# Performance work log

Hardware: AMD Instinct MI355X
Metric: run time of the kernel (lower is better)

Reference implementation:

```python
import jax, jax.numpy as jnp
import numpy as np

BS, N, DX, DE, DY, NH = 4, 256, 256, 64, 128, 8
DF = DX // NH
ORDER = 3


def layer_norm(x, g, b, eps=1e-6):
    m = jnp.mean(x, -1, keepdims=True)
    v = jnp.mean((x - m) ** 2, -1, keepdims=True)
    return (x - m) / jnp.sqrt(v + eps) * g + b


def setup_inputs() -> dict:
    key = jax.random.key(0)
    ks = jax.random.split(key, 32)
    s = 0.02
    p = {}
    p['X'] = jax.random.normal(ks[0], (BS, N, DX), jnp.float32)
    p['E'] = jax.random.normal(ks[1], (BS, N, N, DE), jnp.float32)
    p['y'] = jax.random.normal(ks[2], (BS, DY), jnp.float32)
    lens = jax.random.randint(ks[3], (BS,), N // 2, N + 1)
    p['node_mask'] = (jnp.arange(N)[None, :] < lens[:, None]).astype(jnp.int32)
    p['W_emax'] = s * jax.random.normal(ks[4], (DE, DX))
    p['W_x1'] = s * jax.random.normal(ks[5], (DX, DX))
    p['Wq'] = s * jax.random.normal(ks[6], (DX, DX))
    p['Wk'] = s * jax.random.normal(ks[7], (DX, DX))
    p['Wv'] = s * jax.random.normal(ks[8], (DX, DX))
    p['Wo'] = s * jax.random.normal(ks[9], (DX, DX))
    p['W_y2'] = s * jax.random.normal(ks[10], (DY, DX))
    p['W_x2'] = s * jax.random.normal(ks[11], (DX, DX))
    p['Wc'] = s * jax.random.normal(ks[12], (DY, ORDER))
    p['bc'] = jnp.zeros((ORDER,), jnp.float32)
    p['sim_alpha'] = 0.1 * jax.random.normal(ks[13], (1,))
    p['W_Eout'] = s * jax.random.normal(ks[14], (DE, DE))
    p['G_kernel'] = 0.01 * jax.random.normal(ks[15], (DE, 128))
    p['X_kernel'] = 0.01 * jax.random.normal(ks[16], (DX, 64))
    p['W_Gtrans'] = s * jax.random.normal(ks[17], (128 * DE, DY))
    p['W_Xtrans'] = s * jax.random.normal(ks[18], (64 * DX, DY))
    p['W_yout'] = s * jax.random.normal(ks[19], (DY, DY))
    p['gx'] = jnp.ones((DX,), jnp.float32); p['bx'] = jnp.zeros((DX,), jnp.float32)
    p['ge'] = jnp.ones((DE,), jnp.float32); p['be'] = jnp.zeros((DE,), jnp.float32)
    p['gy'] = jnp.ones((DY,), jnp.float32); p['by'] = jnp.zeros((DY,), jnp.float32)
    return p


def reference(X, E, y, node_mask, W_emax, W_x1, Wq, Wk, Wv, Wo, W_y2, W_x2, Wc, bc,
              sim_alpha, W_Eout, G_kernel, X_kernel, W_Gtrans, W_Xtrans, W_yout,
              gx, bx, ge, be, gy, by):
    bs, n, dx = X.shape
    de = E.shape[-1]
    nm = node_mask.astype(X.dtype)              # bs, n
    x_mask = nm[:, :, None]                     # bs, n, 1
    emask = x_mask[:, :, None, :] * x_mask[:, None, :, :]  # bs, n, n, 1

    # --- edge -> node encoding (masked mean over dim 2; torch mean divides by n) ---
    e_enc = jax.nn.relu(jnp.mean(jnp.einsum('bijd,df->bijf', E, W_emax) * emask, axis=2))
    xplus = (X + jax.nn.relu(e_enc @ W_x1)) * x_mask

    # --- masked multi-head self attention (dropout = identity in eval) ---
    q = (xplus @ Wq).reshape(bs, n, NH, DF)
    k = (xplus @ Wk).reshape(bs, n, NH, DF)
    v = (xplus @ Wv).reshape(bs, n, NH, DF)
    scores = jnp.einsum('bqhd,bkhd->bhqk', q, k) / (DF ** 0.5)
    scores = jnp.where(nm[:, None, None, :] > 0, scores, -1e9)
    attn_out = jnp.einsum('bhqk,bkhd->bqhd', jax.nn.softmax(scores, -1), v).reshape(bs, n, dx) @ Wo
    new_X = layer_norm(attn_out * x_mask + X, gx, bx)

    # --- similarity-augmented edge matrix + order-3 polynomial recurrence ---
    xplusy = jax.nn.relu((X + jax.nn.relu(y @ W_y2)[:, None, :]) @ W_x2)
    sim = jnp.einsum('bnd,bmd->bnm', xplusy, xplusy) / (dx ** 0.5)
    G = (sim_alpha * sim[..., None] + E) * emask          # bs, n, n, de
    Gr = G.reshape(bs, de, n, n)                          # raw reshape, exactly as torch
    coeff = y @ Wc + bc                                    # bs, 3
    newE = coeff[:, 0][:, None, None, None] * Gr
    for kk in range(1, ORDER):
        newE = jnp.matmul(Gr, newE) + coeff[:, kk][:, None, None, None] * Gr
    new_E = layer_norm(jax.nn.relu(newE.reshape(bs, n, n, de) @ W_Eout) * emask + E, ge, be)

    # --- masked softmax pooling over edges ---
    Em = E * emask
    lg = jnp.where(emask > 0, (Em @ G_kernel) / (de ** 0.5), -1e9)   # bs,n,n,128
    aG = jax.nn.softmax(lg.reshape(bs, n * n, -1), axis=1)            # bs,n^2,128
    G_enc = jnp.einsum('bpk,bpd->bkd', aG, Em.reshape(bs, n * n, de)).reshape(bs, -1)
    G_enc = jax.nn.relu(G_enc @ W_Gtrans)

    # --- masked softmax pooling over nodes ---
    Xm = x_mask * X
    lx = jnp.where(x_mask > 0, (Xm @ X_kernel) / (dx ** 0.5), -1e9)   # bs,n,64
    aX = jax.nn.softmax(lx, axis=1)
    X_enc = jnp.einsum('bnk,bnd->bkd', aX, Xm).reshape(bs, -1)
    X_enc = jax.nn.relu(X_enc @ W_Xtrans)

    new_y = layer_norm(jax.nn.relu((G_enc + X_enc) @ W_yout) + y, gy, by)
    return new_X, new_E, new_y
```

## Files before the change

kernel.cpp:

```cpp
#include <hip/hip_runtime.h>
#include <hip/hip_bf16.h>

typedef __hip_bfloat16 bf16;
__device__ __forceinline__ bf16 tobf(float v){ return __float2bfloat16(v); }
__device__ __forceinline__ float frombf(bf16 v){ return __bfloat162float(v); }
__device__ __forceinline__ short f2bs(float x){ bf16 h=tobf(x); return *reinterpret_cast<short*>(&h); }
__device__ __forceinline__ float bs2f(short s){ unsigned int v=((unsigned int)(unsigned short)s)<<16; return __int_as_float((int)v); }

typedef __attribute__((ext_vector_type(8))) short bf16x8;
typedef __attribute__((ext_vector_type(4))) short short4v;
typedef __attribute__((ext_vector_type(4))) float f32x4;
typedef __attribute__((ext_vector_type(4))) int int4v;

static constexpr int cB=4, cN=256, cDX=256, cDE=64, cDY=128, cNH=8, cDF=32;

static constexpr size_t F_SIM  = 0;
static constexpr size_t F_P    = 262144;
static constexpr size_t F_NP   = 2359296;
static constexpr size_t F_GP   = F_NP + 1048576;
static constexpr size_t F_XP   = F_NP + 1048576 + 32768;
static constexpr size_t F_S    = 6619136;
static constexpr size_t F_EENC = 6684672;
static constexpr size_t F_XPL  = 6946816;
static constexpr size_t F_QB   = 7208960;
static constexpr size_t F_KB   = 7471104;
static constexpr size_t F_VB   = 7733248;
static constexpr size_t F_YW   = 7995392;
static constexpr size_t F_XPY  = 7996416;
static constexpr size_t F_COEF = 8258560;
static constexpr size_t F_GENC = 8258576;
static constexpr size_t F_XENC = 8291344;

__global__ void k_coeff_yw(const float* y, const float* Wc, const float* bc,
                           const float* W_y2, float* coeff, float* yw){
  int b = blockIdx.x; int f = threadIdx.x;
  float acc = 0.f;
  for(int r=0;r<cDY;++r) acc += y[b*cDY+r]*W_y2[r*cDX+f];
  yw[b*cDX+f] = fmaxf(acc,0.f);
  if (f < 3){
    float c = bc[f];
    for(int r=0;r<cDY;++r) c += y[b*cDY+r]*Wc[r*3+f];
    coeff[b*3+f] = c;
  }
}

__global__ void k_reduceE(const float* E, const int* nm, float* S){
  int bi = blockIdx.x; int b = bi / cN;
  int d = threadIdx.x;
  int jy = threadIdx.y;
  const float* Eb = E + (size_t)bi*cN*cDE;
  float acc = 0.f;
  for(int j=jy;j<cN;j+=4){
    acc += Eb[j*cDE+d] * (float)nm[b*cN+j];
  }
  __shared__ float red[4][64];
  red[jy][d]=acc; __syncthreads();
  if (jy==0) S[(size_t)bi*cDE+d] = red[0][d]+red[1][d]+red[2][d]+red[3][d];
}

__global__ void k_eenc(const float* S, const float* W_emax, const int* nm, float* eenc){
  int bi = blockIdx.x; int b = bi/cN; int i = bi%cN;
  int f = threadIdx.x;
  __shared__ float s[cDE];
  if (f<cDE) s[f]=S[(size_t)bi*cDE+f];
  __syncthreads();
  float acc=0.f;
  for(int d=0;d<cDE;++d) acc += s[d]*W_emax[d*cDX+f];
  float mi=(float)nm[b*cN+i];
  eenc[(size_t)bi*cDX+f] = fmaxf(acc*mi*(1.f/cN), 0.f);
}

__global__ void k_xplus(const float* X, const float* eenc, const float* W_x1,
                        const int* nm, float* xplus){
  int bi=blockIdx.x; int b=bi/cN; int i=bi%cN;
  int f=threadIdx.x;
  __shared__ float row[cDX];
  row[f]=eenc[(size_t)bi*cDX+f];
  __syncthreads();
  float acc=0.f;
  for(int c=0;c<cDX;++c) acc += row[c]*W_x1[c*cDX+f];
  float mi=(float)nm[b*cN+i];
  xplus[(size_t)bi*cDX+f] = (X[(size_t)bi*cDX+f] + fmaxf(acc,0.f))*mi;
}

__global__ void k_qkv(const float* xplus, const float* Wq, const float* Wk, const float* Wv,
                      float* qb, float* kb, float* vb){
  int bi=blockIdx.x; int f=threadIdx.x;
  __shared__ float row[cDX];
  row[f]=xplus[(size_t)bi*cDX+f];
  __syncthreads();
  float aq=0,ak=0,av=0;
  for(int c=0;c<cDX;++c){ float r=row[c]; aq+=r*Wq[c*cDX+f]; ak+=r*Wk[c*cDX+f]; av+=r*Wv[c*cDX+f]; }
  qb[(size_t)bi*cDX+f]=aq; kb[(size_t)bi*cDX+f]=ak; vb[(size_t)bi*cDX+f]=av;
}

__global__ void k_attn_softmax(const float* qb, const float* kb, const int* nm, float* P){
  int id=blockIdx.x; int b=id/(cNH*cN); int rem=id%(cNH*cN); int h=rem/cN; int i=rem%cN;
  int j=threadIdx.x;
  __shared__ float qrow[cDF];
  if (j<cDF) qrow[j]=qb[((size_t)b*cN+i)*cDX + h*cDF + j];
  __syncthreads();
  const float* krow = kb + ((size_t)b*cN+j)*cDX + h*cDF;
  float s=0.f;
  for(int c=0;c<cDF;++c) s += qrow[c]*krow[c];
  s *= 0.17677669529663687f;
  float val = (nm[b*cN+j]>0) ? s : -1e9f;
  __shared__ float red[256];
  red[j]=val; __syncthreads();
  for(int st=128;st>0;st>>=1){ if(j<st) red[j]=fmaxf(red[j],red[j+st]); __syncthreads(); }
  float mx=red[0]; __syncthreads();
  float e=__expf(val-mx);
  red[j]=e; __syncthreads();
  for(int st=128;st>0;st>>=1){ if(j<st) red[j]+=red[j+st]; __syncthreads(); }
  float denom=red[0];
  P[(size_t)id*cN + j] = e/denom;
}

__global__ void k_attn_out(const float* P, const float* vb, const float* Wo,
                           const float* X, const int* nm, const float* gx, const float* bx,
                           float* newX){
  int bi=blockIdx.x; int b=bi/cN; int i=bi%cN;
  int t=threadIdx.x;
  __shared__ float p8[cNH][cN];
  for(int h=0;h<cNH;++h) p8[h][t]=P[(((size_t)b*cNH+h)*cN+i)*cN + t];
  __syncthreads();
  int h=t/cDF;
  float acc=0.f;
  for(int j=0;j<cN;++j) acc += p8[h][j]*vb[((size_t)b*cN+j)*cDX + t];
  __shared__ float arow[cDX];
  arow[t]=acc; __syncthreads();
  float o=0.f;
  for(int c=0;c<cDX;++c) o += arow[c]*Wo[c*cDX+t];
  float mi=(float)nm[b*cN+i];
  float v = o*mi + X[(size_t)bi*cDX+t];
  __shared__ float red[256];
  red[t]=v; __syncthreads();
  for(int st=128;st>0;st>>=1){ if(t<st) red[t]+=red[t+st]; __syncthreads(); }
  float mean=red[0]*(1.f/cDX); __syncthreads();
  float dv=v-mean;
  red[t]=dv*dv; __syncthreads();
  for(int st=128;st>0;st>>=1){ if(t<st) red[t]+=red[t+st]; __syncthreads(); }
  float var=red[0]*(1.f/cDX);
  newX[(size_t)bi*cDX+t]=dv*rsqrtf(var+1e-6f)*gx[t]+bx[t];
}

__global__ void k_xplusy(const float* X, const float* yw, const float* W_x2, float* xpy){
  int bi=blockIdx.x; int b=bi/cN;
  int f=threadIdx.x;
  __shared__ float row[cDX];
  row[f]=X[(size_t)bi*cDX+f]+yw[b*cDX+f];
  __syncthreads();
  float acc=0.f;
  for(int c=0;c<cDX;++c) acc += row[c]*W_x2[c*cDX+f];
  xpy[(size_t)bi*cDX+f]=fmaxf(acc,0.f);
}

__global__ void k_sim(const float* xp, float* sim){
  int b=blockIdx.z;
  int tx=threadIdx.x, ty=threadIdx.y;
  __shared__ float Aa[16][17], Bb[16][17];
  const float* base = xp + (size_t)b*cN*cDX;
  float acc=0.f;
  for(int kt=0;kt<cDX;kt+=16){
    Aa[ty][tx]=base[(size_t)(blockIdx.y*16+ty)*cDX + kt+tx];
    Bb[ty][tx]=base[(size_t)(blockIdx.x*16+ty)*cDX + kt+tx];
    __syncthreads();
    for(int c=0;c<16;++c) acc += Aa[ty][c]*Bb[tx][c];
    __syncthreads();
  }
  sim[((size_t)b*cN + blockIdx.y*16+ty)*cN + blockIdx.x*16+tx] = acc*(1.f/16.f);
}

__global__ void k_G(const float* E, const float* sim, const int* nm, const float* alpha_p,
                    bf16* G){
  int bi=blockIdx.x; int b=bi/cN; int i=bi%cN;
  float mi=(float)nm[b*cN+i];
  float alpha=alpha_p[0];
  size_t base=(size_t)bi*cN*cDE;
  for(int t=threadIdx.x;t<cN*cDE;t+=blockDim.x){
    int j=t>>6;
    float mj=(float)nm[b*cN+j];
    G[base+t]=tobf((alpha*sim[(size_t)bi*cN+j]+E[base+t])*mi*mj);
  }
}

__global__ void __launch_bounds__(256) k_transp(const short* G, short* Gt){
  const int bc=blockIdx.z;
  const int p0=blockIdx.y*128, q0=blockIdx.x*128;
  const int t=threadIdx.x;
  __shared__ short T[128][136];
  const short* src=G+(size_t)bc*65536;
  short* dst=Gt+(size_t)bc*65536;
#pragma unroll
  for(int l=0;l<8;++l){
    int idx=t+l*256;
    int r=idx>>4, seg=idx&15;
    *(int4v*)&T[r][seg*8]=*(const int4v*)&src[(size_t)(p0+r)*256 + q0 + seg*8];
  }
  __syncthreads();
  int qq=t&127, hf=t>>7;
#pragma unroll
  for(int ss=0;ss<8;++ss){
    bf16x8 v;
#pragma unroll
    for(int ii=0;ii<8;++ii) v[ii]=T[hf*64+ss*8+ii][qq];
    *(bf16x8*)&dst[(size_t)(q0+qq)*256 + p0 + hf*64 + ss*8]=v;
  }
}

__global__ void __launch_bounds__(256) k_bmm_t(const short* G, const short* Gt, short* Bt2,
                                               const float* coeff){
  const int bc=blockIdx.z; const int b=bc>>6;
  const float alpha=coeff[b*3+0];
  const float beta=coeff[b*3+1];
  const short* Ag=G+(size_t)bc*65536;
  const short* At=Gt+(size_t)bc*65536;
  short* Ct=Bt2+(size_t)bc*65536;
  const int row0=blockIdx.y*128, col0=blockIdx.x*128;
  const int t=threadIdx.x;
  const int lane=t&63, w=t>>6;
  const int wr=w>>1, wc=w&1;
  const int l15=lane&15, l4=lane>>4;
  __shared__ char smem[36864];
  short (*A_s)[72]=(short(*)[72])smem;
  short (*B_s)[72]=(short(*)[72])(smem+18432);
  float (*Cf)[132]=(float(*)[132])smem;
  f32x4 acc[4][4];
#pragma unroll
  for(int m=0;m<4;++m)
#pragma unroll
    for(int n=0;n<4;++n) acc[m][n]=(f32x4){0.f,0.f,0.f,0.f};

  for(int kt=0;kt<256;kt+=64){
#pragma unroll
    for(int l=0;l<4;++l){
      int idx=t+l*256;
      int r=idx>>3, seg=idx&7;
      *(int4v*)&A_s[r][seg*8]=*(const int4v*)&Ag[(size_t)(row0+r)*256 + kt + seg*8];
      *(int4v*)&B_s[r][seg*8]=*(const int4v*)&At[(size_t)(col0+r)*256 + kt + seg*8];
    }
    __syncthreads();
#pragma unroll
    for(int ks=0;ks<64;ks+=32){
      bf16x8 am[4], bn[4];
#pragma unroll
      for(int m=0;m<4;++m) am[m]=*(const bf16x8*)&A_s[wr*64+m*16+l15][ks+l4*8];
#pragma unroll
      for(int n=0;n<4;++n) bn[n]=*(const bf16x8*)&B_s[wc*64+n*16+l15][ks+l4*8];
#pragma unroll
      for(int m=0;m<4;++m)
#pragma unroll
        for(int n=0;n<4;++n)
          acc[m][n]=__builtin_amdgcn_mfma_f32_16x16x32_bf16(am[m],bn[n],acc[m][n],0,0,0);
    }
    __syncthreads();
  }
  for(int rs=0;rs<8;++rs){
    if(rs) __syncthreads();
    int m=rs&3;
    if(wr==(rs>>2)){
#pragma unroll
      for(int n=0;n<4;++n)
#pragma unroll
        for(int r=0;r<4;++r)
          Cf[l4*4+r][wc*64+n*16+l15]=acc[m][n][r];
    }
    __syncthreads();
    int c=t&127, hf=t>>7;
    const short* gsrc=&At[(size_t)(col0+c)*256 + row0 + rs*16 + hf*8];
    short* dst=&Ct[(size_t)(col0+c)*256 + row0 + rs*16 + hf*8];
    bf16x8 a8=*(const bf16x8*)gsrc;
    bf16x8 o8;
#pragma unroll
    for(int ii=0;ii<8;++ii)
      o8[ii]=f2bs(alpha*Cf[hf*8+ii][c] + beta*bs2f(a8[ii]));
    *(bf16x8*)dst=o8;
  }
}

__global__ void __launch_bounds__(256) k_bmm_f(const short* G, const short* Bt2, float* C,
                                               const float* coeff){
  const int bc=blockIdx.z; const int b=bc>>6;
  const float beta=coeff[b*3+2];
  const short* Ag=G+(size_t)bc*65536;
  const short* Bt=Bt2+(size_t)bc*65536;
  float* Cb=C+(size_t)bc*65536;
  const int row0=blockIdx.y*128, col0=blockIdx.x*128;
  const int t=threadIdx.x;
  const int lane=t&63, w=t>>6;
  const int wr=w>>1, wc=w&1;
  const int l15=lane&15, l4=lane>>4;
  __shared__ char smem[36864];
  short (*A_s)[72]=(short(*)[72])smem;
  short (*B_s)[72]=(short(*)[72])(smem+18432);
  float (*Cf)[132]=(float(*)[132])smem;
  f32x4 acc[4][4];
#pragma unroll
  for(int m=0;m<4;++m)
#pragma unroll
    for(int n=0;n<4;++n) acc[m][n]=(f32x4){0.f,0.f,0.f,0.f};

  for(int kt=0;kt<256;kt+=64){
#pragma unroll
    for(int l=0;l<4;++l){
      int idx=t+l*256;
      int r=idx>>3, seg=idx&7;
      *(int4v*)&A_s[r][seg*8]=*(const int4v*)&Ag[(size_t)(row0+r)*256 + kt + seg*8];
      *(int4v*)&B_s[r][seg*8]=*(const int4v*)&Bt[(size_t)(col0+r)*256 + kt + seg*8];
    }
    __syncthreads();
#pragma unroll
    for(int ks=0;ks<64;ks+=32){
      bf16x8 am[4], bn[4];
#pragma unroll
      for(int m=0;m<4;++m) am[m]=*(const bf16x8*)&A_s[wr*64+m*16+l15][ks+l4*8];
#pragma unroll
      for(int n=0;n<4;++n) bn[n]=*(const bf16x8*)&B_s[wc*64+n*16+l15][ks+l4*8];
#pragma unroll
      for(int m=0;m<4;++m)
#pragma unroll
        for(int n=0;n<4;++n)
          acc[m][n]=__builtin_amdgcn_mfma_f32_16x16x32_bf16(am[m],bn[n],acc[m][n],0,0,0);
    }
    __syncthreads();
  }
  for(int rs=0;rs<8;++rs){
    if(rs) __syncthreads();
    int m=rs&3;
    if(wr==(rs>>2)){
#pragma unroll
      for(int n=0;n<4;++n)
#pragma unroll
        for(int r=0;r<4;++r)
          Cf[l4*4+r][wc*64+n*16+l15]=acc[m][n][r];
    }
    __syncthreads();
    int r=t>>4, cs=t&15;
    int row=row0+rs*16+r;
    const short* asrc=&Ag[(size_t)row*256 + col0 + cs*8];
    float* dst=&Cb[(size_t)row*256 + col0 + cs*8];
    bf16x8 a8=*(const bf16x8*)asrc;
    f32x4 o0,o1;
#pragma unroll
    for(int ii=0;ii<4;++ii) o0[ii]=Cf[r][cs*8+ii]   + beta*bs2f(a8[ii]);
#pragma unroll
    for(int ii=0;ii<4;++ii) o1[ii]=Cf[r][cs*8+4+ii] + beta*bs2f(a8[4+ii]);
    *(f32x4*)&dst[0]=o0;
    *(f32x4*)&dst[4]=o1;
  }
}

__global__ void __launch_bounds__(256) k_Eout_mfma(const float* newE_in, const float* E,
                       const int* nm, const float* W_Eout, const float* ge, const float* be,
                       float* outE){
  const int t=threadIdx.x;
  const int lane=t&63, w=t>>6;
  const int l15=lane&15, l4=lane>>4;
  const int blk=blockIdx.x;
  const int b=blk>>8, i=blk&255;
  const float mi=(float)nm[b*cN+i];
  bf16x8 bnf[2][4];
#pragma unroll
  for(int ks=0;ks<2;++ks)
#pragma unroll
    for(int n=0;n<4;++n){
      bf16x8 v;
#pragma unroll
      for(int ii=0;ii<8;++ii)
        v[ii]=f2bs(W_Eout[(ks*32+l4*8+ii)*cDE + n*16+l15]);
      bnf[ks][n]=v;
    }
  float gev[4], bev[4];
#pragma unroll
  for(int n=0;n<4;++n){ gev[n]=ge[n*16+l15]; bev[n]=be[n*16+l15]; }

  for(int it=0;it<4;++it){
    const int j0=it*64+w*16;
    const int p0=blk*256 + j0;
    f32x4 acc[4];
#pragma unroll
    for(int n=0;n<4;++n) acc[n]=(f32x4){0.f,0.f,0.f,0.f};
    if(mi>0.f){
#pragma unroll
      for(int ks=0;ks<2;++ks){
        const float* ap=&newE_in[(size_t)(p0+l15)*cDE + ks*32 + l4*8];
        float4 a0=*(const float4*)ap;
        float4 a1=*(const float4*)(ap+4);
        bf16x8 am;
        am[0]=f2bs(a0.x); am[1]=f2bs(a0.y); am[2]=f2bs(a0.z); am[3]=f2bs(a0.w);
        am[4]=f2bs(a1.x); am[5]=f2bs(a1.y); am[6]=f2bs(a1.z); am[7]=f2bs(a1.w);
#pragma unroll
        for(int n=0;n<4;++n)
          acc[n]=__builtin_amdgcn_mfma_f32_16x16x32_bf16(am,bnf[ks][n],acc[n],0,0,0);
      }
    }
    float mj[4];
#pragma unroll
    for(int r=0;r<4;++r) mj[r]=mi*(float)nm[b*cN + j0 + l4*4 + r];
#pragma unroll
    for(int reg=0;reg<4;++reg){
      size_t rowoff=(size_t)(p0 + l4*4 + reg)*cDE;
      float v0=fmaxf(acc[0][reg],0.f)*mj[reg]+E[rowoff + 0*16+l15];
      float v1=fmaxf(acc[1][reg],0.f)*mj[reg]+E[rowoff + 1*16+l15];
      float v2=fmaxf(acc[2][reg],0.f)*mj[reg]+E[rowoff + 2*16+l15];
      float v3=fmaxf(acc[3][reg],0.f)*mj[reg]+E[rowoff + 3*16+l15];
      float s=v0+v1+v2+v3;
      float q=v0*v0+v1*v1+v2*v2+v3*v3;
#pragma unroll
      for(int m=1;m<16;m<<=1){ s+=__shfl_xor(s,m); q+=__shfl_xor(q,m); }
      float mean=s*(1.f/cDE);
      float var=q*(1.f/cDE)-mean*mean;
      float inv=rsqrtf(var+1e-6f);
      outE[rowoff + 0*16+l15]=(v0-mean)*inv*gev[0]+bev[0];
      outE[rowoff + 1*16+l15]=(v1-mean)*inv*gev[1]+bev[1];
      outE[rowoff + 2*16+l15]=(v2-mean)*inv*gev[2]+bev[2];
      outE[rowoff + 3*16+l15]=(v3-mean)*inv*gev[3]+bev[3];
    }
  }
}

__global__ void __launch_bounds__(256) k_Gaccum_mfma(const float* E, const int* nm,
                                                     const float* G_kernel,
                                                     float* Npart, float* Dpart){
  const int chunk=blockIdx.x;
  const int b=blockIdx.y;
  const int t=threadIdx.x;
  const int lane=t&63, w=t>>6;
  const int l15=lane&15, l4=lane>>4;

  __shared__ short EmA[128][72];
  __shared__ short EmT[64][136];
  __shared__ short Wt[128][136];
  __shared__ float mrow[128];
  __shared__ float Dacc[128];
  __shared__ float Dpar[4][128];

  bf16x8 gk[2][8];
#pragma unroll
  for(int kt=0;kt<2;++kt)
#pragma unroll
    for(int n=0;n<8;++n){
      bf16x8 v;
#pragma unroll
      for(int ii=0;ii<8;++ii)
        v[ii]=f2bs(G_kernel[(kt*32+l4*8+ii)*128 + n*16+l15]*0.125f);
      gk[kt][n]=v;
    }

  f32x4 nacc[2][4];
#pragma unroll
  for(int a=0;a<2;++a)
#pragma unroll
    for(int d2=0;d2<4;++d2) nacc[a][d2]=(f32x4){0.f,0.f,0.f,0.f};

  if(t<128) Dacc[t]=0.f;
  __syncthreads();

  const size_t ebase=((size_t)b)<<16;
  for(int sub=0;sub<4;++sub){
    const int rowbase = chunk*512 + sub*128;
    {
      int pr=t>>1, hh=t&1;
      int p=rowbase+pr;
      const float* src=&E[(ebase+p)*cDE + hh*32];
#pragma unroll
      for(int q=0;q<8;++q){
        float4 v=*(const float4*)(src+q*4);
        short4v s4; s4[0]=f2bs(v.x); s4[1]=f2bs(v.y); s4[2]=f2bs(v.z); s4[3]=f2bs(v.w);
        *(short4v*)&EmA[pr][hh*32+q*4]=s4;
        EmT[hh*32+q*4+0][pr]=s4[0];
        EmT[hh*32+q*4+1][pr]=s4[1];
        EmT[hh*32+q*4+2][pr]=s4[2];
        EmT[hh*32+q*4+3][pr]=s4[3];
      }
      if(hh==0) mrow[pr]=(float)(nm[b*cN+(p>>8)]*nm[b*cN+(p&255)]);
    }
    __syncthreads();

    f32x4 wacc[2][8];
#pragma unroll
    for(int m=0;m<2;++m)
#pragma unroll
      for(int n=0;n<8;++n) wacc[m][n]=(f32x4){0.f,0.f,0.f,0.f};
#pragma unroll
    for(int kt=0;kt<2;++kt){
      bf16x8 am[2];
#pragma unroll
      for(int m=0;m<2;++m) am[m]=*(const bf16x8*)&EmA[w*32+m*16+l15][kt*32+l4*8];
#pragma unroll
      for(int m=0;m<2;++m)
#pragma unroll
        for(int n=0;n<8;++n)
          wacc[m][n]=__builtin_amdgcn_mfma_f32_16x16x32_bf16(am[m],gk[kt][n],wacc[m][n],0,0,0);
    }
    float dsum[8];
#pragma unroll
    for(int n=0;n<8;++n) dsum[n]=0.f;
#pragma unroll
    for(int m=0;m<2;++m){
#pragma unroll
      for(int r=0;r<4;++r){
        int pl=w*32+m*16+l4*4+r;
        float mv=mrow[pl];
#pragma unroll
        for(int n=0;n<8;++n){
          float wv=(mv>0.f)?__expf(wacc[m][n][r]):0.f;
          dsum[n]+=wv;
          Wt[n*16+l15][pl]=f2bs(wv);
        }
      }
    }
#pragma unroll
    for(int n=0;n<8;++n){
      float s=dsum[n];
      s+=__shfl_xor(s,16); s+=__shfl_xor(s,32);
      if(l4==0) Dpar[w][n*16+l15]=s;
    }
    __syncthreads();

#pragma unroll
    for(int ks=0;ks<4;++ks){
      bf16x8 aw[2];
#pragma unroll
      for(int a=0;a<2;++a) aw[a]=*(const bf16x8*)&Wt[w*32+a*16+l15][ks*32+l4*8];
      bf16x8 bm[4];
#pragma unroll
      for(int d2=0;d2<4;++d2)
        bm[d2]=*(const bf16x8*)&EmT[d2*16+l15][ks*32+l4*8];
#pragma unroll
      for(int a=0;a<2;++a)
#pragma unroll
        for(int d2=0;d2<4;++d2)
          nacc[a][d2]=__builtin_amdgcn_mfma_f32_16x16x32_bf16(aw[a],bm[d2],nacc[a][d2],0,0,0);
    }
    __syncthreads();
    if(t<128) Dacc[t]+=Dpar[0][t]+Dpar[1][t]+Dpar[2][t]+Dpar[3][t];
    __syncthreads();
  }

  size_t pi=(size_t)b*128+chunk;
  float* np=Npart + pi*128*cDE;
#pragma unroll
  for(int a=0;a<2;++a){
#pragma unroll
    for(int d2=0;d2<4;++d2){
#pragma unroll
      for(int r=0;r<4;++r){
        int k=w*32+a*16+l4*4+r;
        int d=d2*16+l15;
        np[(size_t)k*cDE+d]=nacc[a][d2][r];
      }
    }
  }
  if(t<128) Dpart[pi*128+t]=Dacc[t];
}

__global__ void k_Gcombine(const float* Npart, const float* Dpart, float* Genc){
  int bk=blockIdx.x; int b=bk>>7; int k=bk&127;
  int d=threadIdx.x;
  float n=0.f, dd=0.f;
  for(int pi=0;pi<128;++pi){
    size_t base=((size_t)b*128+pi)*128+k;
    n += Npart[base*cDE+d];
    dd += Dpart[base];
  }
  Genc[(size_t)b*8192 + k*cDE + d]=n/dd;
}

__global__ void k_Xenc(const float* X, const int* nm, const float* X_kernel, float* Xenc){
  int k=blockIdx.x;
  int b=blockIdx.y;
  int n=threadIdx.x;
  float m=(float)nm[b*cN+n];
  const float* xr=X+((size_t)b*cN+n)*cDX;
  float acc=0.f;
  for(int c=0;c<cDX;++c) acc += xr[c]*X_kernel[c*64+k];
  float lg=(m>0.f)?acc*(1.f/16.f):-1e9f;
  __shared__ float red[256];
  red[n]=lg; __syncthreads();
  for(int st=128;st>0;st>>=1){ if(n<st) red[n]=fmaxf(red[n],red[n+st]); __syncthreads(); }
  float mx=red[0]; __syncthreads();
  float e=__expf(lg-mx);
  red[n]=e; __syncthreads();
  for(int st=128;st>0;st>>=1){ if(n<st) red[n]+=red[n+st]; __syncthreads(); }
  float denom=red[0]; __syncthreads();
  __shared__ float ps[256];
  ps[n]=e/denom;
  __syncthreads();
  int d=n;
  float s=0.f;
  for(int nn=0;nn<cN;++nn) s += ps[nn]*X[((size_t)b*cN+nn)*cDX+d];
  Xenc[(size_t)b*16384 + k*cDX + d]=s;
}

__global__ void __launch_bounds__(256) k_headA(const float* Genc, const float* Xenc,
                        const float* W_Gtrans, const float* W_Xtrans,
                        float* Gp, float* Xp){
  int blk=blockIdx.x;
  int t=threadIdx.x;
  int o=t&127, sub=t>>7;
  int b0=sub*2, b1=sub*2+1;
  __shared__ float ash[4][128];
  if(blk<64){
    int ch=blk;
    for(int l=t;l<512;l+=256){
      int b=l>>7, q=l&127;
      ash[b][q]=Genc[(size_t)b*8192 + ch*128 + q];
    }
    __syncthreads();
    const float* wbase=W_Gtrans + (size_t)ch*128*cDY + o;
    float a0=0.f, a1=0.f;
#pragma unroll 4
    for(int qq=0;qq<128;++qq){
      float w=wbase[(size_t)qq*cDY];
      a0+=ash[b0][qq]*w; a1+=ash[b1][qq]*w;
    }
    Gp[((size_t)b0*64+ch)*cDY+o]=a0;
    Gp[((size_t)b1*64+ch)*cDY+o]=a1;
  } else {
    int ch=blk-64;
    for(int l=t;l<512;l+=256){
      int b=l>>7, q=l&127;
      ash[b][q]=Xenc[(size_t)b*16384 + ch*128 + q];
    }
    __syncthreads();
    const float* wbase=W_Xtrans + (size_t)ch*128*cDY + o;
    float a0=0.f, a1=0.f;
#pragma unroll 4
    for(int qq=0;qq<128;++qq){
      float w=wbase[(size_t)qq*cDY];
      a0+=ash[b0][qq]*w; a1+=ash[b1][qq]*w;
    }
    Xp[((size_t)b0*128+ch)*cDY+o]=a0;
    Xp[((size_t)b1*128+ch)*cDY+o]=a1;
  }
}

__global__ void k_headB(const float* Gp, const float* Xp, const float* W_yout,
                        const float* y, const float* gy, const float* by, float* newy){
  int b=blockIdx.x; int o=threadIdx.x;
  float g=0.f,x=0.f;
  for(int ch=0;ch<64;++ch)  g+=Gp[((size_t)b*64+ch)*cDY+o];
  for(int ch=0;ch<128;++ch) x+=Xp[((size_t)b*128+ch)*cDY+o];
  __shared__ float srow[cDY];
  srow[o]=fmaxf(g,0.f)+fmaxf(x,0.f);
  __syncthreads();
  float h=0.f;
  for(int r=0;r<cDY;++r) h += srow[r]*W_yout[r*cDY+o];
  float v=fmaxf(h,0.f)+y[b*cDY+o];
  __shared__ float red[cDY];
  red[o]=v; __syncthreads();
  for(int st=64;st>0;st>>=1){ if(o<st) red[o]+=red[o+st]; __syncthreads(); }
  float mean=red[0]*(1.f/cDY); __syncthreads();
  float dv=v-mean;
  red[o]=dv*dv; __syncthreads();
  for(int st=64;st>0;st>>=1){ if(o<st) red[o]+=red[o+st]; __syncthreads(); }
  float var=red[0]*(1.f/cDY);
  newy[b*cDY+o]=dv*rsqrtf(var+1e-6f)*gy[o]+by[o];
}

extern "C" void kernel_launch(void* const* d_in, const int* in_sizes, int n_in,
                              void* d_out, int out_size, void* d_ws, size_t ws_size,
                              hipStream_t stream){
  const float* X     =(const float*)d_in[0];
  const float* E     =(const float*)d_in[1];
  const float* y     =(const float*)d_in[2];
  const int*   nm    =(const int*)  d_in[3];
  const float* W_emax=(const float*)d_in[4];
  const float* W_x1  =(const float*)d_in[5];
  const float* Wq    =(const float*)d_in[6];
  const float* Wk    =(const float*)d_in[7];
  const float* Wv    =(const float*)d_in[8];
  const float* Wo    =(const float*)d_in[9];
  const float* W_y2  =(const float*)d_in[10];
  const float* W_x2  =(const float*)d_in[11];
  const float* Wc    =(const float*)d_in[12];
  const float* bc    =(const float*)d_in[13];
  const float* salpha=(const float*)d_in[14];
  const float* W_Eout=(const float*)d_in[15];
  const float* G_kern=(const float*)d_in[16];
  const float* X_kern=(const float*)d_in[17];
  const float* W_Gtr =(const float*)d_in[18];
  const float* W_Xtr =(const float*)d_in[19];
  const float* W_yout=(const float*)d_in[20];
  const float* gx    =(const float*)d_in[21];
  const float* bx    =(const float*)d_in[22];
  const float* ge    =(const float*)d_in[23];
  const float* be    =(const float*)d_in[24];
  const float* gy    =(const float*)d_in[25];
  const float* by    =(const float*)d_in[26];

  char* wsb=(char*)d_ws;
  bf16* Gbf=(bf16*)wsb;
  short* Gs=(short*)wsb;
  short* Bt2=(short*)(wsb+33554432);
  short* Gts=(short*)(wsb+67108864);
  float* Npart=(float*)(wsb+33554432);
  float* f32=(float*)(wsb+100663296);
  float* sim  = f32+F_SIM;
  float* P    = f32+F_P;
  float* Dpart= f32+F_NP;
  float* Gp   = f32+F_GP;
  float* Xp   = f32+F_XP;
  float* S    = f32+F_S;
  float* eenc = f32+F_EENC;
  float* xplus= f32+F_XPL;
  float* qb   = f32+F_QB;
  float* kb   = f32+F_KB;
  float* vb   = f32+F_VB;
  float* yw   = f32+F_YW;
  float* xpy  = f32+F_XPY;
  float* coeff= f32+F_COEF;
  float* Genc = f32+F_GENC;
  float* Xenc = f32+F_XENC;

  float* out=(float*)d_out;
  float* newX=out;
  float* newE_out=out+262144;
  float* newy=out+17039360;

  k_coeff_yw<<<cB,256,0,stream>>>(y,Wc,bc,W_y2,coeff,yw);
  k_reduceE<<<cB*cN,dim3(64,4),0,stream>>>(E,nm,S);
  k_eenc<<<cB*cN,256,0,stream>>>(S,W_emax,nm,eenc);
  k_xplus<<<cB*cN,256,0,stream>>>(X,eenc,W_x1,nm,xplus);
  k_qkv<<<cB*cN,256,0,stream>>>(xplus,Wq,Wk,Wv,qb,kb,vb);
  k_attn_softmax<<<cB*cNH*cN,256,0,stream>>>(qb,kb,nm,P);
  k_attn_out<<<cB*cN,256,0,stream>>>(P,vb,Wo,X,nm,gx,bx,newX);
  k_xplusy<<<cB*cN,256,0,stream>>>(X,yw,W_x2,xpy);
  k_sim<<<dim3(16,16,cB),dim3(16,16),0,stream>>>(xpy,sim);
  k_G<<<cB*cN,256,0,stream>>>(E,sim,nm,salpha,Gbf);
  k_transp<<<dim3(2,2,cB*cDE),256,0,stream>>>(Gs,Gts);
  k_bmm_t<<<dim3(2,2,cB*cDE),256,0,stream>>>(Gs,Gts,Bt2,coeff);
  k_bmm_f<<<dim3(2,2,cB*cDE),256,0,stream>>>(Gs,Bt2,newE_out,coeff);
  k_Eout_mfma<<<1024,256,0,stream>>>(newE_out,E,nm,W_Eout,ge,be,newE_out);
  k_Gaccum_mfma<<<dim3(128,cB),256,0,stream>>>(E,nm,G_kern,Npart,Dpart);
  k_Gcombine<<<cB*128,64,0,stream>>>(Npart,Dpart,Genc);
  k_Xenc<<<dim3(64,cB),256,0,stream>>>(X,nm,X_kern,Xenc);
  k_headA<<<192,256,0,stream>>>(Genc,Xenc,W_Gtr,W_Xtr,Gp,Xp);
  k_headB<<<cB,128,0,stream>>>(Gp,Xp,W_yout,y,gy,by,newy);
}
```

Before: 413.1 us.

## Store bmm_f result as bf16 intermediate and remap transpose-store thread indexing

The final batched matmul now writes its output as bf16 into a workspace buffer (reusing the Gts region) instead of fp32 into the output tensor, and the Eout kernel reads bf16 directly, since it converted to bf16 anyway. This halves the intermediate write and read traffic of a 16M-element tensor. Separately, the k_bmm_t epilogue changes its thread-to-column mapping so adjacent threads write adjacent 16-byte chunks of the same row, improving coalescing. It relies on Gts being dead after k_bmm_t.

```diff
diff --git a/kernel.cpp b/kernel.cpp
--- a/kernel.cpp
+++ b/kernel.cpp
@@ -266,7 +266,7 @@
           Cf[l4*4+r][wc*64+n*16+l15]=acc[m][n][r];
     }
     __syncthreads();
-    int c=t&127, hf=t>>7;
+    int c=t>>1, hf=t&1;
     const short* gsrc=&At[(size_t)(col0+c)*256 + row0 + rs*16 + hf*8];
     short* dst=&Ct[(size_t)(col0+c)*256 + row0 + rs*16 + hf*8];
     bf16x8 a8=*(const bf16x8*)gsrc;
@@ -278,13 +278,13 @@
   }
 }
 
-__global__ void __launch_bounds__(256) k_bmm_f(const short* G, const short* Bt2, float* C,
+__global__ void __launch_bounds__(256) k_bmm_f(const short* G, const short* Bt2, short* Cbf,
                                                const float* coeff){
   const int bc=blockIdx.z; const int b=bc>>6;
   const float beta=coeff[b*3+2];
   const short* Ag=G+(size_t)bc*65536;
   const short* Bt=Bt2+(size_t)bc*65536;
-  float* Cb=C+(size_t)bc*65536;
+  short* Cb=Cbf+(size_t)bc*65536;
   const int row0=blockIdx.y*128, col0=blockIdx.x*128;
   const int t=threadIdx.x;
   const int lane=t&63, w=t>>6;
@@ -338,19 +338,17 @@
     int r=t>>4, cs=t&15;
     int row=row0+rs*16+r;
     const short* asrc=&Ag[(size_t)row*256 + col0 + cs*8];
-    float* dst=&Cb[(size_t)row*256 + col0 + cs*8];
+    short* dst=&Cb[(size_t)row*256 + col0 + cs*8];
     bf16x8 a8=*(const bf16x8*)asrc;
-    f32x4 o0,o1;
-#pragma unroll
-    for(int ii=0;ii<4;++ii) o0[ii]=Cf[r][cs*8+ii]   + beta*bs2f(a8[ii]);
-#pragma unroll
-    for(int ii=0;ii<4;++ii) o1[ii]=Cf[r][cs*8+4+ii] + beta*bs2f(a8[4+ii]);
-    *(f32x4*)&dst[0]=o0;
-    *(f32x4*)&dst[4]=o1;
-  }
-}
-
-__global__ void __launch_bounds__(256) k_Eout_mfma(const float* newE_in, const float* E,
+    bf16x8 o8;
+#pragma unroll
+    for(int ii=0;ii<8;++ii)
+      o8[ii]=f2bs(Cf[r][cs*8+ii] + beta*bs2f(a8[ii]));
+    *(bf16x8*)dst=o8;
+  }
+}
+
+__global__ void __launch_bounds__(256) k_Eout_mfma(const short* newE_in, const float* E,
                        const int* nm, const float* W_Eout, const float* ge, const float* be,
                        float* outE){
   const int t=threadIdx.x;
@@ -383,12 +381,7 @@
     if(mi>0.f){
 #pragma unroll
       for(int ks=0;ks<2;++ks){
-        const float* ap=&newE_in[(size_t)(p0+l15)*cDE + ks*32 + l4*8];
-        float4 a0=*(const float4*)ap;
-        float4 a1=*(const float4*)(ap+4);
-        bf16x8 am;
-        am[0]=f2bs(a0.x); am[1]=f2bs(a0.y); am[2]=f2bs(a0.z); am[3]=f2bs(a0.w);
-        am[4]=f2bs(a1.x); am[5]=f2bs(a1.y); am[6]=f2bs(a1.z); am[7]=f2bs(a1.w);
+        bf16x8 am=*(const bf16x8*)&newE_in[(size_t)(p0+l15)*cDE + ks*32 + l4*8];
 #pragma unroll
         for(int n=0;n<4;++n)
           acc[n]=__builtin_amdgcn_mfma_f32_16x16x32_bf16(am,bnf[ks][n],acc[n],0,0,0);
@@ -695,6 +688,7 @@
   short* Gs=(short*)wsb;
   short* Bt2=(short*)(wsb+33554432);
   short* Gts=(short*)(wsb+67108864);
+  short* NEWEbf=(short*)(wsb+67108864);
   float* Npart=(float*)(wsb+33554432);
   float* f32=(float*)(wsb+100663296);
   float* sim  = f32+F_SIM;
@@ -731,8 +725,8 @@
   k_G<<<cB*cN,256,0,stream>>>(E,sim,nm,salpha,Gbf);
   k_transp<<<dim3(2,2,cB*cDE),256,0,stream>>>(Gs,Gts);
   k_bmm_t<<<dim3(2,2,cB*cDE),256,0,stream>>>(Gs,Gts,Bt2,coeff);
-  k_bmm_f<<<dim3(2,2,cB*cDE),256,0,stream>>>(Gs,Bt2,newE_out,coeff);
-  k_Eout_mfma<<<1024,256,0,stream>>>(newE_out,E,nm,W_Eout,ge,be,newE_out);
+  k_bmm_f<<<dim3(2,2,cB*cDE),256,0,stream>>>(Gs,Bt2,NEWEbf,coeff);
+  k_Eout_mfma<<<1024,256,0,stream>>>(NEWEbf,E,nm,W_Eout,ge,be,newE_out);
   k_Gaccum_mfma<<<dim3(128,cB),256,0,stream>>>(E,nm,G_kern,Npart,Dpart);
   k_Gcombine<<<cB*128,64,0,stream>>>(Npart,Dpart,Genc);
   k_Xenc<<<dim3(64,cB),256,0,stream>>>(X,nm,X_kern,Xenc);
```

Result: faster. 390.1 us (-5.6%).
